# Kernel tuning notes

Measured on AMD Instinct MI355X. Metric: run time of the kernel, lower is better.

Reference implementation:

```python
import jax, jax.numpy as jnp
import numpy as np

NPG = 100          # nodes per graph
NUM_GRAPHS = 500
N = NPG * NUM_GRAPHS
DEG = 32
E = N * DEG
IN_DIM = 100
HID = 64           # out_channels / hidden_dim
HEADS = 2
NCLS = 2


def setup_inputs() -> dict:
    key = jax.random.key(0)
    ks = jax.random.split(key, 24)
    rng = np.random.default_rng(0)
    # edges within each graph, guaranteed no self-loops
    dst = np.repeat(np.arange(N), DEG)
    off = rng.integers(1, NPG, size=E)
    src = (dst // NPG) * NPG + ((dst % NPG) + off) % NPG
    edge_index = jnp.asarray(np.stack([src, dst]).astype(np.int32))
    batch = jnp.asarray((np.arange(N) // NPG).astype(np.int32))
    HC = HEADS * HID
    p = lambda k, sh: jax.random.normal(k, sh, jnp.float32) * 0.1
    return dict(
        x=jax.random.normal(ks[0], (N, IN_DIM), jnp.float32),
        edge_attr=jax.random.uniform(ks[1], (E,), jnp.float32),
        W1=p(ks[2], (IN_DIM, HC)), as1=p(ks[3], (HEADS, HID)), ad1=p(ks[4], (HEADS, HID)), bg1=p(ks[5], (HC,)),
        l1W=p(ks[6], (HC, HID)), l1b=p(ks[7], (HID,)), g1=jnp.ones((HID,), jnp.float32), b1=jnp.zeros((HID,), jnp.float32),
        W2=p(ks[8], (HID, HC)), as2=p(ks[9], (HEADS, HID)), ad2=p(ks[10], (HEADS, HID)), bg2=p(ks[11], (HC,)),
        l2W=p(ks[12], (HC, HID)), l2b=p(ks[13], (HID,)), g2=jnp.ones((HID,), jnp.float32), b2=jnp.zeros((HID,), jnp.float32),
        f1W=p(ks[14], (HID, HID)), f1b=p(ks[15], (HID,)),
        f2W=p(ks[16], (HID, HID // 2)), f2b=p(ks[17], (HID // 2,)),
        f3W=p(ks[18], (HID // 2, NCLS)), f3b=p(ks[19], (NCLS,)),
        edge_index=edge_index, batch=batch)


def reference(x, edge_attr, W1, as1, ad1, bg1, l1W, l1b, g1, b1,
              W2, as2, ad2, bg2, l2W, l2b, g2, b2,
              f1W, f1b, f2W, f2b, f3W, f3b, edge_index, batch):
    n = x.shape[0]
    ea = jnp.abs(edge_attr)  # computed as in forward; unused by attention_weighted variant
    # GATConv adds self-loops (fill doesn't matter for alpha-only message)
    sl = jnp.arange(n, dtype=edge_index.dtype)
    src = jnp.concatenate([edge_index[0], sl])
    dst = jnp.concatenate([edge_index[1], sl])
    lrelu = lambda z: jax.nn.leaky_relu(z, 0.2)

    def gat(h, W, a_s, a_d, bias):
        xp = (h @ W).reshape(n, HEADS, HID)                 # [N,H,C]
        e = lrelu(jnp.sum(xp * a_s, -1)[src] + jnp.sum(xp * a_d, -1)[dst])  # [E',H]
        m = jax.ops.segment_max(e, dst, num_segments=n)
        ex = jnp.exp(e - m[dst])
        alpha = ex / jax.ops.segment_sum(ex, dst, num_segments=n)[dst]      # edge softmax per dst
        out = jax.ops.segment_sum(xp[src] * alpha[:, :, None], dst, num_segments=n)
        return out.reshape(n, HEADS * HID) + bias

    def bn(z, g, b):  # BatchNorm1d with batch statistics (biased var, eps=1e-5)
        return (z - z.mean(0)) * jax.lax.rsqrt(z.var(0) + 1e-5) * g + b

    z = bn(lrelu(gat(x, W1, as1, ad1, bg1) @ l1W + l1b), g1, b1)
    z = bn(lrelu(gat(z, W2, as2, ad2, bg2) @ l2W + l2b), g2, b2)
    # global mean pool
    s = jax.ops.segment_sum(z, batch, num_segments=NUM_GRAPHS)
    cnt = jax.ops.segment_sum(jnp.ones((n, 1), z.dtype), batch, num_segments=NUM_GRAPHS)
    z = s / cnt
    z = lrelu(z @ f1W + f1b)
    z = lrelu(z @ f2W + f2b)
    return z @ f3W + f3b
```

## Files before the change

kernel.cpp:

```cpp
#include <hip/hip_runtime.h>

#define NN 50000
#define NPGc 100
#define NG 500
#define DEG 32
#define HC 128
#define HID 64

__device__ __forceinline__ float lrelu(float x) { return x > 0.0f ? x : 0.2f * x; }

__global__ void k_prep(const float* __restrict__ W1, const float* __restrict__ as1,
                       const float* __restrict__ ad1, float* __restrict__ Wa1,
                       const float* __restrict__ W2, const float* __restrict__ as2,
                       const float* __restrict__ ad2, float* __restrict__ Wa2) {
  const float* W  = blockIdx.x ? W2 : W1;
  const float* as_ = blockIdx.x ? as2 : as1;
  const float* ad_ = blockIdx.x ? ad2 : ad1;
  float* Wa = blockIdx.x ? Wa2 : Wa1;
  int K = blockIdx.x ? 64 : 100;
  int t = threadIdx.x;
  for (int u = t; u < K * 4; u += blockDim.x) {
    int k = u >> 2, s = u & 3;
    const float* a = (s < 2) ? as_ : ad_;
    int h = s & 1;
    float acc = 0.f;
    for (int c = 0; c < 64; ++c) acc += W[k * 128 + h * 64 + c] * a[h * 64 + c];
    Wa[k * 4 + s] = acc;
  }
}

template <int K, bool BN>
__global__ __launch_bounds__(256) void k_in_gemm(
    const float* __restrict__ in, const float* __restrict__ W,
    const float* __restrict__ Wa, const float* __restrict__ AB,
    float* __restrict__ xp, float* __restrict__ ssrc, float* __restrict__ sdst) {
  constexpr int KP = (K % 8 == 0) ? K + 4 : K;
  __shared__ __align__(16) float xs[64 * KP];
  int t = threadIdx.x;
  int n0 = blockIdx.x * 64;

  constexpr int RQ = K / 4;
  for (int u = t; u < 64 * RQ; u += 256) {
    int r = u / RQ, q = u % RQ;
    int n = n0 + r;
    float4 v = make_float4(0.f, 0.f, 0.f, 0.f);
    if (n < NN) v = ((const float4*)(in + (size_t)n * K))[q];
    if (BN) {
      float4 a4 = ((const float4*)AB)[q];
      float4 b4 = ((const float4*)(AB + 64))[q];
      v.x = v.x * a4.x + b4.x; v.y = v.y * a4.y + b4.y;
      v.z = v.z * a4.z + b4.z; v.w = v.w * a4.w + b4.w;
    }
    ((float4*)(xs + r * KP))[q] = v;
  }
  __syncthreads();

  int ng = t >> 5, cg = t & 31;
  int r0 = ng * 8;
  float4 acc[8];
#pragma unroll
  for (int i = 0; i < 8; ++i) acc[i] = make_float4(0.f, 0.f, 0.f, 0.f);

  const float4* W4 = (const float4*)W;
  float4 w4 = W4[cg];
  for (int k = 0; k < K; ++k) {
    float4 wc = w4;
    if (k + 1 < K) w4 = W4[(k + 1) * 32 + cg];
#pragma unroll
    for (int i = 0; i < 8; ++i) {
      float a = xs[(r0 + i) * KP + k];
      acc[i].x += a * wc.x; acc[i].y += a * wc.y;
      acc[i].z += a * wc.z; acc[i].w += a * wc.w;
    }
  }
#pragma unroll
  for (int i = 0; i < 8; ++i) {
    int n = n0 + r0 + i;
    if (n < NN) ((float4*)(xp + (size_t)n * HC))[cg] = acc[i];
  }
  {
    int r = t >> 2, s = t & 3;
    float sc = 0.f;
    for (int k = 0; k < K; ++k) sc += xs[r * KP + k] * Wa[k * 4 + s];
    int n = n0 + r;
    if (n < NN) {
      if (s < 2) ssrc[n * 2 + s] = sc;
      else       sdst[n * 2 + (s - 2)] = sc;
    }
  }
}

__global__ __launch_bounds__(256) void k_gat(
    const float* __restrict__ xp, const float* __restrict__ ssrc,
    const float* __restrict__ sdst, const int* __restrict__ esrc,
    const float* __restrict__ bg, float* __restrict__ out) {
  __shared__ __align__(16) float xl[NPGc * 64];
  __shared__ float sh[NPGc];
  __shared__ float sdh[NPGc];
  __shared__ unsigned short srcl[NPGc * DEG];
  __shared__ float alpha[NPGc * (DEG + 2)];
  int t = threadIdx.x;
  int g = blockIdx.x >> 1, h = blockIdx.x & 1;
  int base = g * NPGc;

  const float4* xp4 = (const float4*)(xp + (size_t)base * HC);
  for (int u = t; u < NPGc * 16; u += 256)
    ((float4*)xl)[u] = xp4[(u >> 4) * 32 + h * 16 + (u & 15)];
  if (t < NPGc) {
    sh[t] = ssrc[(base + t) * 2 + h];
    sdh[t] = sdst[(base + t) * 2 + h];
  }
  for (int u = t; u < NPGc * DEG; u += 256)
    srcl[u] = (unsigned short)(esrc[base * DEG + u] - base);
  __syncthreads();

  if (t < NPGc) {
    float sd = sdh[t];
    float es = lrelu(sh[t] + sd);
    float m = es;
    float e[DEG];
#pragma unroll
    for (int j = 0; j < DEG; ++j) {
      e[j] = lrelu(sh[srcl[t * DEG + j]] + sd);
      m = fmaxf(m, e[j]);
    }
    float exs = __expf(es - m);
    float den = exs;
#pragma unroll
    for (int j = 0; j < DEG; ++j) { e[j] = __expf(e[j] - m); den += e[j]; }
    float inv = 1.0f / den;
    float* al = alpha + t * (DEG + 2);
#pragma unroll
    for (int j = 0; j < DEG; ++j) al[j] = e[j] * inv;
    al[DEG] = exs * inv;
  }
  __syncthreads();

  int c4 = t & 15;
  float4 bgv = ((const float4*)bg)[h * 16 + c4];
  for (int d = t >> 4; d < NPGc; d += 16) {
    const float* al = alpha + d * (DEG + 2);
    const unsigned short* sp = srcl + d * DEG;
    float aself = al[DEG];
    float4 x4 = ((float4*)xl)[d * 16 + c4];
    float4 acc;
    acc.x = aself * x4.x; acc.y = aself * x4.y;
    acc.z = aself * x4.z; acc.w = aself * x4.w;
#pragma unroll 8
    for (int j = 0; j < DEG; ++j) {
      float a = al[j];
      float4 v = ((float4*)xl)[(int)sp[j] * 16 + c4];
      acc.x += a * v.x; acc.y += a * v.y;
      acc.z += a * v.z; acc.w += a * v.w;
    }
    acc.x += bgv.x; acc.y += bgv.y; acc.z += bgv.z; acc.w += bgv.w;
    ((float4*)out)[(size_t)(base + d) * 32 + h * 16 + c4] = acc;
  }
}

__global__ __launch_bounds__(256) void k_out_gemm(
    const float* __restrict__ gin, const float* __restrict__ lW,
    const float* __restrict__ lb, float* __restrict__ h,
    float* __restrict__ partial) {
  __shared__ __align__(16) float gl[64 * 132];
  __shared__ float psum[2 * HID];
  int t = threadIdx.x;
  int n0 = blockIdx.x * 64;

  for (int u = t; u < 64 * 32; u += 256) {
    int r = u >> 5, q = u & 31;
    int n = n0 + r;
    float4 v = make_float4(0.f, 0.f, 0.f, 0.f);
    if (n < NN) v = ((const float4*)(gin + (size_t)n * HC))[q];
    ((float4*)(gl + r * 132))[q] = v;
  }
  if (t < 2 * HID) psum[t] = 0.f;
  __syncthreads();

  int ng = t >> 4, cg = t & 15;
  int r0 = ng * 4;
  float4 acc[4];
#pragma unroll
  for (int i = 0; i < 4; ++i) acc[i] = make_float4(0.f, 0.f, 0.f, 0.f);

  const float4* lW4 = (const float4*)lW;
  float4 w4 = lW4[cg];
  for (int k = 0; k < HC; ++k) {
    float4 wc = w4;
    if (k + 1 < HC) w4 = lW4[(k + 1) * 16 + cg];
#pragma unroll
    for (int i = 0; i < 4; ++i) {
      float a = gl[(r0 + i) * 132 + k];
      acc[i].x += a * wc.x; acc[i].y += a * wc.y;
      acc[i].z += a * wc.z; acc[i].w += a * wc.w;
    }
  }
  float4 bias = ((const float4*)lb)[cg];
  float s0 = 0, s1 = 0, s2 = 0, s3 = 0, q0 = 0, q1 = 0, q2 = 0, q3 = 0;
#pragma unroll
  for (int i = 0; i < 4; ++i) {
    int n = n0 + r0 + i;
    if (n < NN) {
      float4 v;
      v.x = lrelu(acc[i].x + bias.x); v.y = lrelu(acc[i].y + bias.y);
      v.z = lrelu(acc[i].z + bias.z); v.w = lrelu(acc[i].w + bias.w);
      ((float4*)(h + (size_t)n * HID))[cg] = v;
      s0 += v.x; q0 += v.x * v.x; s1 += v.y; q1 += v.y * v.y;
      s2 += v.z; q2 += v.z * v.z; s3 += v.w; q3 += v.w * v.w;
    }
  }
  int c0 = cg * 4;
  atomicAdd(&psum[c0 + 0], s0); atomicAdd(&psum[c0 + 1], s1);
  atomicAdd(&psum[c0 + 2], s2); atomicAdd(&psum[c0 + 3], s3);
  atomicAdd(&psum[HID + c0 + 0], q0); atomicAdd(&psum[HID + c0 + 1], q1);
  atomicAdd(&psum[HID + c0 + 2], q2); atomicAdd(&psum[HID + c0 + 3], q3);
  __syncthreads();
  if (t < 2 * HID) partial[blockIdx.x * 128 + t] = psum[t];
}

__global__ __launch_bounds__(256) void k_stats(
    const float* __restrict__ partial, int nb, const float* __restrict__ gamma,
    const float* __restrict__ beta, float* __restrict__ AB) {
  __shared__ float red[2][256];
  int c = blockIdx.x, t = threadIdx.x;
  float s = 0.f, sq = 0.f;
  for (int i = t; i < nb; i += 256) {
    s += partial[i * 128 + c];
    sq += partial[i * 128 + 64 + c];
  }
  red[0][t] = s; red[1][t] = sq;
  __syncthreads();
  for (int o = 128; o > 0; o >>= 1) {
    if (t < o) { red[0][t] += red[0][t + o]; red[1][t] += red[1][t + o]; }
    __syncthreads();
  }
  if (t == 0) {
    float mean = red[0][0] / (float)NN;
    float var = red[1][0] / (float)NN - mean * mean;
    float A = gamma[c] * rsqrtf(var + 1e-5f);
    AB[c] = A;
    AB[64 + c] = beta[c] - mean * A;
  }
}

__global__ __launch_bounds__(64) void k_pool_mlp(
    const float* __restrict__ h2, const float* __restrict__ AB,
    const float* __restrict__ f1W, const float* __restrict__ f1b,
    const float* __restrict__ f2W, const float* __restrict__ f2b,
    const float* __restrict__ f3W, const float* __restrict__ f3b,
    float* __restrict__ out) {
  __shared__ float pp[4 * 64];
  __shared__ float pooled[64];
  __shared__ float z1[64];
  __shared__ float z2[32];
  int g = blockIdx.x, t = threadIdx.x;
  const float4* hb4 = (const float4*)(h2 + (size_t)g * NPGc * HID);
  int rq = t >> 4, c4 = t & 15;
  float4 s4 = make_float4(0.f, 0.f, 0.f, 0.f);
  for (int r = rq; r < NPGc; r += 4) {
    float4 v = hb4[r * 16 + c4];
    s4.x += v.x; s4.y += v.y; s4.z += v.z; s4.w += v.w;
  }
  ((float4*)pp)[rq * 16 + c4] = s4;
  __syncthreads();
  pooled[t] = (pp[t] + pp[64 + t] + pp[128 + t] + pp[192 + t]) * (1.0f / NPGc) * AB[t] + AB[64 + t];
  __syncthreads();
  float a = f1b[t];
  for (int c = 0; c < 64; ++c) a += pooled[c] * f1W[c * 64 + t];
  z1[t] = lrelu(a);
  __syncthreads();
  if (t < 32) {
    float a2 = f2b[t];
    for (int c = 0; c < 64; ++c) a2 += z1[c] * f2W[c * 32 + t];
    z2[t] = lrelu(a2);
  }
  __syncthreads();
  if (t < 2) {
    float a3 = f3b[t];
    for (int c = 0; c < 32; ++c) a3 += z2[c] * f3W[c * 2 + t];
    out[g * 2 + t] = a3;
  }
}

extern "C" void kernel_launch(void* const* d_in, const int* in_sizes, int n_in,
                              void* d_out, int out_size, void* d_ws, size_t ws_size,
                              hipStream_t stream) {
  const float* x   = (const float*)d_in[0];
  const float* W1  = (const float*)d_in[2];
  const float* as1 = (const float*)d_in[3];
  const float* ad1 = (const float*)d_in[4];
  const float* bg1 = (const float*)d_in[5];
  const float* l1W = (const float*)d_in[6];
  const float* l1b = (const float*)d_in[7];
  const float* g1  = (const float*)d_in[8];
  const float* b1  = (const float*)d_in[9];
  const float* W2  = (const float*)d_in[10];
  const float* as2 = (const float*)d_in[11];
  const float* ad2 = (const float*)d_in[12];
  const float* bg2 = (const float*)d_in[13];
  const float* l2W = (const float*)d_in[14];
  const float* l2b = (const float*)d_in[15];
  const float* g2  = (const float*)d_in[16];
  const float* b2  = (const float*)d_in[17];
  const float* f1W = (const float*)d_in[18];
  const float* f1b = (const float*)d_in[19];
  const float* f2W = (const float*)d_in[20];
  const float* f2b = (const float*)d_in[21];
  const float* f3W = (const float*)d_in[22];
  const float* f3b = (const float*)d_in[23];
  const int* esrc  = (const int*)d_in[24];
  float* out = (float*)d_out;

  float* ws = (float*)d_ws;
  size_t off = 0;
  auto alloc = [&](size_t nf) { float* p = ws + off; off += (nf + 63) & ~(size_t)63; return p; };
  float* Wa1     = alloc(100 * 4);
  float* Wa2     = alloc(64 * 4);
  float* xp      = alloc((size_t)NN * HC);
  float* ssrc    = alloc((size_t)NN * 2);
  float* sdst    = alloc((size_t)NN * 2);
  float* gout    = alloc((size_t)NN * HC);
  float* hbuf    = alloc((size_t)NN * HID);
  const int NB = (NN + 63) / 64;
  float* partial = alloc((size_t)NB * 128);
  float* AB1     = alloc(128);
  float* AB2     = alloc(128);
  (void)in_sizes; (void)n_in; (void)out_size; (void)ws_size;

  k_prep<<<2, 256, 0, stream>>>(W1, as1, ad1, Wa1, W2, as2, ad2, Wa2);
  k_in_gemm<100, false><<<NB, 256, 0, stream>>>(x, W1, Wa1, nullptr, xp, ssrc, sdst);
  k_gat<<<NG * 2, 256, 0, stream>>>(xp, ssrc, sdst, esrc, bg1, gout);
  k_out_gemm<<<NB, 256, 0, stream>>>(gout, l1W, l1b, hbuf, partial);
  k_stats<<<64, 256, 0, stream>>>(partial, NB, g1, b1, AB1);
  k_in_gemm<64, true><<<NB, 256, 0, stream>>>(hbuf, W2, Wa2, AB1, xp, ssrc, sdst);
  k_gat<<<NG * 2, 256, 0, stream>>>(xp, ssrc, sdst, esrc, bg2, gout);
  k_out_gemm<<<NB, 256, 0, stream>>>(gout, l2W, l2b, hbuf, partial);
  k_stats<<<64, 256, 0, stream>>>(partial, NB, g2, b2, AB2);
  k_pool_mlp<<<NG, 64, 0, stream>>>(hbuf, AB2, f1W, f1b, f2W, f2b, f3W, f3b, out);
}
```

Before: 320.7 us.

## Fuse input projection GEMM and attention scores into per-graph GAT kernel

Merges the input GEMM (xp projection and attention scores) with the GAT aggregation kernel, so each block (one graph, one head) computes its projected features directly into shared memory. This removes the global round trip of the N×128 xp buffer and the score arrays, plus one launch per layer. In exchange each block reads its graph's full input rows twice (once per head) and uses shared memory aliasing for scratch buffers, which could lower occupancy.

```diff
diff --git a/kernel.cpp b/kernel.cpp
--- a/kernel.cpp
+++ b/kernel.cpp
@@ -30,98 +30,83 @@
 }
 
 template <int K, bool BN>
-__global__ __launch_bounds__(256) void k_in_gemm(
+__global__ __launch_bounds__(256) void k_layer(
     const float* __restrict__ in, const float* __restrict__ W,
     const float* __restrict__ Wa, const float* __restrict__ AB,
-    float* __restrict__ xp, float* __restrict__ ssrc, float* __restrict__ sdst) {
-  constexpr int KP = (K % 8 == 0) ? K + 4 : K;
-  __shared__ __align__(16) float xs[64 * KP];
+    const int* __restrict__ esrc, const float* __restrict__ bg,
+    float* __restrict__ gout) {
+  constexpr int KP = (K % 32 == 0) ? K + 4 : K;
+  __shared__ __align__(16) float xph[NPGc * 64];
+  __shared__ __align__(16) char ubuf[NPGc * KP * 4];
+  float* xin = (float*)ubuf;
+  unsigned short* srcl = (unsigned short*)ubuf;
+  float* sc = (float*)(ubuf + 6400);
+  float* alpha = (float*)(ubuf + 7232);
+
   int t = threadIdx.x;
-  int n0 = blockIdx.x * 64;
+  int g = blockIdx.x >> 1, h = blockIdx.x & 1;
+  int base = g * NPGc;
 
   constexpr int RQ = K / 4;
-  for (int u = t; u < 64 * RQ; u += 256) {
+  for (int u = t; u < NPGc * RQ; u += 256) {
     int r = u / RQ, q = u % RQ;
-    int n = n0 + r;
-    float4 v = make_float4(0.f, 0.f, 0.f, 0.f);
-    if (n < NN) v = ((const float4*)(in + (size_t)n * K))[q];
+    float4 v = ((const float4*)(in + (size_t)(base + r) * K))[q];
     if (BN) {
       float4 a4 = ((const float4*)AB)[q];
       float4 b4 = ((const float4*)(AB + 64))[q];
       v.x = v.x * a4.x + b4.x; v.y = v.y * a4.y + b4.y;
       v.z = v.z * a4.z + b4.z; v.w = v.w * a4.w + b4.w;
     }
-    ((float4*)(xs + r * KP))[q] = v;
-  }
-  __syncthreads();
-
-  int ng = t >> 5, cg = t & 31;
-  int r0 = ng * 8;
-  float4 acc[8];
-#pragma unroll
-  for (int i = 0; i < 8; ++i) acc[i] = make_float4(0.f, 0.f, 0.f, 0.f);
-
-  const float4* W4 = (const float4*)W;
-  float4 w4 = W4[cg];
-  for (int k = 0; k < K; ++k) {
-    float4 wc = w4;
-    if (k + 1 < K) w4 = W4[(k + 1) * 32 + cg];
-#pragma unroll
-    for (int i = 0; i < 8; ++i) {
-      float a = xs[(r0 + i) * KP + k];
-      acc[i].x += a * wc.x; acc[i].y += a * wc.y;
-      acc[i].z += a * wc.z; acc[i].w += a * wc.w;
-    }
-  }
-#pragma unroll
-  for (int i = 0; i < 8; ++i) {
-    int n = n0 + r0 + i;
-    if (n < NN) ((float4*)(xp + (size_t)n * HC))[cg] = acc[i];
-  }
+    ((float4*)(xin + r * KP))[q] = v;
+  }
+  __syncthreads();
+
+  int ng = t >> 4, cg = t & 15;
   {
-    int r = t >> 2, s = t & 3;
-    float sc = 0.f;
-    for (int k = 0; k < K; ++k) sc += xs[r * KP + k] * Wa[k * 4 + s];
-    int n = n0 + r;
-    if (n < NN) {
-      if (s < 2) ssrc[n * 2 + s] = sc;
-      else       sdst[n * 2 + (s - 2)] = sc;
-    }
-  }
-}
-
-__global__ __launch_bounds__(256) void k_gat(
-    const float* __restrict__ xp, const float* __restrict__ ssrc,
-    const float* __restrict__ sdst, const int* __restrict__ esrc,
-    const float* __restrict__ bg, float* __restrict__ out) {
-  __shared__ __align__(16) float xl[NPGc * 64];
-  __shared__ float sh[NPGc];
-  __shared__ float sdh[NPGc];
-  __shared__ unsigned short srcl[NPGc * DEG];
-  __shared__ float alpha[NPGc * (DEG + 2)];
-  int t = threadIdx.x;
-  int g = blockIdx.x >> 1, h = blockIdx.x & 1;
-  int base = g * NPGc;
-
-  const float4* xp4 = (const float4*)(xp + (size_t)base * HC);
-  for (int u = t; u < NPGc * 16; u += 256)
-    ((float4*)xl)[u] = xp4[(u >> 4) * 32 + h * 16 + (u & 15)];
-  if (t < NPGc) {
-    sh[t] = ssrc[(base + t) * 2 + h];
-    sdh[t] = sdst[(base + t) * 2 + h];
-  }
+    float4 acc[7];
+#pragma unroll
+    for (int i = 0; i < 7; ++i) acc[i] = make_float4(0.f, 0.f, 0.f, 0.f);
+    const float4* W4 = (const float4*)W;
+    float4 w4 = W4[h * 16 + cg];
+    for (int k = 0; k < K; ++k) {
+      float4 wc = w4;
+      if (k + 1 < K) w4 = W4[(k + 1) * 32 + h * 16 + cg];
+#pragma unroll
+      for (int i = 0; i < 7; ++i) {
+        int r = ng + 16 * i;
+        if (r < NPGc) {
+          float a = xin[r * KP + k];
+          acc[i].x += a * wc.x; acc[i].y += a * wc.y;
+          acc[i].z += a * wc.z; acc[i].w += a * wc.w;
+        }
+      }
+    }
+#pragma unroll
+    for (int i = 0; i < 7; ++i) {
+      int r = ng + 16 * i;
+      if (r < NPGc) ((float4*)xph)[r * 16 + cg] = acc[i];
+    }
+  }
+  float myscore = 0.f;
+  if (t < 200) {
+    int node = t >> 1, s = t & 1;
+    for (int k = 0; k < K; ++k) myscore += xin[node * KP + k] * Wa[k * 4 + s * 2 + h];
+  }
+  __syncthreads();
+
+  if (t < 200) sc[(t & 1) * NPGc + (t >> 1)] = myscore;
   for (int u = t; u < NPGc * DEG; u += 256)
     srcl[u] = (unsigned short)(esrc[base * DEG + u] - base);
   __syncthreads();
 
   if (t < NPGc) {
-    float sd = sdh[t];
-    float es = lrelu(sh[t] + sd);
+    float sd = sc[NPGc + t];
+    float es = lrelu(sc[t] + sd);
     float m = es;
     float e[DEG];
 #pragma unroll
     for (int j = 0; j < DEG; ++j) {
-      e[j] = lrelu(sh[srcl[t * DEG + j]] + sd);
+      e[j] = lrelu(sc[srcl[t * DEG + j]] + sd);
       m = fmaxf(m, e[j]);
     }
     float exs = __expf(es - m);
@@ -136,25 +121,24 @@
   }
   __syncthreads();
 
-  int c4 = t & 15;
-  float4 bgv = ((const float4*)bg)[h * 16 + c4];
-  for (int d = t >> 4; d < NPGc; d += 16) {
+  float4 bgv = ((const float4*)bg)[h * 16 + cg];
+  for (int d = ng; d < NPGc; d += 16) {
     const float* al = alpha + d * (DEG + 2);
     const unsigned short* sp = srcl + d * DEG;
     float aself = al[DEG];
-    float4 x4 = ((float4*)xl)[d * 16 + c4];
+    float4 x4 = ((float4*)xph)[d * 16 + cg];
     float4 acc;
     acc.x = aself * x4.x; acc.y = aself * x4.y;
     acc.z = aself * x4.z; acc.w = aself * x4.w;
 #pragma unroll 8
     for (int j = 0; j < DEG; ++j) {
       float a = al[j];
-      float4 v = ((float4*)xl)[(int)sp[j] * 16 + c4];
+      float4 v = ((float4*)xph)[(int)sp[j] * 16 + cg];
       acc.x += a * v.x; acc.y += a * v.y;
       acc.z += a * v.z; acc.w += a * v.w;
     }
     acc.x += bgv.x; acc.y += bgv.y; acc.z += bgv.z; acc.w += bgv.w;
-    ((float4*)out)[(size_t)(base + d) * 32 + h * 16 + c4] = acc;
+    ((float4*)gout)[(size_t)(base + d) * 32 + h * 16 + cg] = acc;
   }
 }
 
@@ -316,9 +300,6 @@
   auto alloc = [&](size_t nf) { float* p = ws + off; off += (nf + 63) & ~(size_t)63; return p; };
   float* Wa1     = alloc(100 * 4);
   float* Wa2     = alloc(64 * 4);
-  float* xp      = alloc((size_t)NN * HC);
-  float* ssrc    = alloc((size_t)NN * 2);
-  float* sdst    = alloc((size_t)NN * 2);
   float* gout    = alloc((size_t)NN * HC);
   float* hbuf    = alloc((size_t)NN * HID);
   const int NB = (NN + 63) / 64;
@@ -328,12 +309,10 @@
   (void)in_sizes; (void)n_in; (void)out_size; (void)ws_size;
 
   k_prep<<<2, 256, 0, stream>>>(W1, as1, ad1, Wa1, W2, as2, ad2, Wa2);
-  k_in_gemm<100, false><<<NB, 256, 0, stream>>>(x, W1, Wa1, nullptr, xp, ssrc, sdst);
-  k_gat<<<NG * 2, 256, 0, stream>>>(xp, ssrc, sdst, esrc, bg1, gout);
+  k_layer<100, false><<<NG * 2, 256, 0, stream>>>(x, W1, Wa1, nullptr, esrc, bg1, gout);
   k_out_gemm<<<NB, 256, 0, stream>>>(gout, l1W, l1b, hbuf, partial);
   k_stats<<<64, 256, 0, stream>>>(partial, NB, g1, b1, AB1);
-  k_in_gemm<64, true><<<NB, 256, 0, stream>>>(hbuf, W2, Wa2, AB1, xp, ssrc, sdst);
-  k_gat<<<NG * 2, 256, 0, stream>>>(xp, ssrc, sdst, esrc, bg2, gout);
+  k_layer<64, true><<<NG * 2, 256, 0, stream>>>(hbuf, W2, Wa2, AB1, esrc, bg2, gout);
   k_out_gemm<<<NB, 256, 0, stream>>>(gout, l2W, l2b, hbuf, partial);
   k_stats<<<64, 256, 0, stream>>>(partial, NB, g2, b2, AB2);
   k_pool_mlp<<<NG, 64, 0, stream>>>(hbuf, AB2, f1W, f1b, f2W, f2b, f3W, f3b, out);
```

Result: slower. 344.2 us (+7.4%).
